# Kernel optimization log

Hardware: AMD Instinct MI355X
Metric: run time of the kernel (lower is better)

## Reference

```python
import jax, jax.numpy as jnp
import numpy as np

EPS = 1e-5

def group_norm(x, gamma, beta, groups):
    # x: (B, C, D, H, W)
    B, C = x.shape[0], x.shape[1]
    xr = x.reshape(B, groups, C // groups, -1)
    mean = xr.mean(axis=(2, 3), keepdims=True)
    var = xr.var(axis=(2, 3), keepdims=True)
    xn = ((xr - mean) * jax.lax.rsqrt(var + EPS)).reshape(x.shape)
    return xn * gamma[None, :, None, None, None] + beta[None, :, None, None, None]

def setup_inputs() -> dict:
    key = jax.random.key(0)
    ks = jax.random.split(key, 8)
    B, Ccls = 2, 32
    D = H = W = 64
    s = 0.05
    return {
        "x": jax.random.normal(ks[0], (B, 768, 8, 8, 8), jnp.float32),
        "out": jax.random.normal(ks[1], (B, 48, D, H, W), jnp.float32),
        "task_encoding": jax.random.normal(ks[2], (Ccls, 256, 1, 1, 1), jnp.float32),
        "gn1_g": jnp.ones((768,), jnp.float32),
        "gn1_b": jnp.zeros((768,), jnp.float32),
        "gap_w": jax.random.normal(ks[3], (256, 768), jnp.float32) * s,
        "gap_b": jnp.zeros((256,), jnp.float32),
        "ctrl_w": jax.random.normal(ks[4], (153, 512), jnp.float32) * s,
        "ctrl_b": jnp.zeros((153,), jnp.float32),
        "gn2_g": jnp.ones((48,), jnp.float32),
        "gn2_b": jnp.zeros((48,), jnp.float32),
        "pre_w": jax.random.normal(ks[5], (8, 48), jnp.float32) * s,
        "pre_b": jnp.zeros((8,), jnp.float32),
    }

def reference(x, out, task_encoding, gn1_g, gn1_b, gap_w, gap_b, ctrl_w, ctrl_b,
              gn2_g, gn2_b, pre_w, pre_b):
    B = x.shape[0]
    Ccls = task_encoding.shape[0]
    # GAP branch: GroupNorm(16,768) -> ReLU -> global avg pool -> 1x1x1 conv 768->256
    h = jax.nn.relu(group_norm(x, gn1_g, gn1_b, 16))
    pooled = h.mean(axis=(2, 3, 4))                       # (B, 768)
    x_feat = pooled @ gap_w.T + gap_b                     # (B, 256)
    # Controller: per (batch, class) params from concat(x_feat, task_encoding)
    te = task_encoding.reshape(Ccls, -1)                  # (Ccls, 256)
    params = (jnp.einsum('pf,bf->bp', ctrl_w[:, :256], x_feat)[:, None, :]
              + jnp.einsum('pf,cf->cp', ctrl_w[:, 256:], te)[None, :, :]
              + ctrl_b)                                   # (B, Ccls, 153)
    w1 = params[..., 0:64].reshape(B, Ccls, 8, 8)
    w2 = params[..., 64:128].reshape(B, Ccls, 8, 8)
    w3 = params[..., 128:136].reshape(B, Ccls, 1, 8)
    b1 = params[..., 136:144]
    b2 = params[..., 144:152]
    b3 = params[..., 152:153]
    # precls branch: GroupNorm(16,48) -> ReLU -> 1x1x1 conv 48->8
    g = jax.nn.relu(group_norm(out, gn2_g, gn2_b, 16))
    h0 = jnp.einsum('oc,bcdhw->bodhw', pre_w, g) + pre_b[None, :, None, None, None]
    # Dynamic per-class head: 8->8->8->1 pointwise MLP with ReLU between layers
    t = jax.nn.relu(jnp.einsum('bcij,bjdhw->bcidhw', w1, h0) + b1[..., None, None, None])
    t = jax.nn.relu(jnp.einsum('bcij,bcjdhw->bcidhw', w2, t) + b2[..., None, None, None])
    logits = jnp.einsum('bcij,bcjdhw->bcidhw', w3, t) + b3[..., None, None, None]
    # (B, Ccls, 1, D, H, W) -> (B, Ccls, D, H, W)
    return logits[:, :, 0]
```

## Files before the change

kernel.cpp:

```cpp
#include <hip/hip_runtime.h>

constexpr int NCLS = 32;

constexpr int WS_POOL = 64;
constexpr int WS_XF  = 1600;
constexpr int WS_PAR = 2112;
constexpr int WS_P2  = 11904;

__device__ __forceinline__ float wred(float v) {
#pragma unroll
  for (int off = 32; off > 0; off >>= 1) v += __shfl_down(v, off, 64);
  return v;
}

__device__ __forceinline__ float2 fma2(float w, float2 v, float2 a) {
  a.x = fmaf(w, v.x, a.x); a.y = fmaf(w, v.y, a.y);
  return a;
}
__device__ __forceinline__ float2 relu2(float2 a) {
  a.x = fmaxf(a.x, 0.f); a.y = fmaxf(a.y, 0.f);
  return a;
}
__device__ __forceinline__ float2 bcast2(float v) { return make_float2(v, v); }

__global__ void k1_stats(const float* __restrict__ x, const float* __restrict__ oin,
                         const float* __restrict__ g1, const float* __restrict__ b1,
                         float* __restrict__ ws) {
  int t = threadIdx.x;
  int wid = t >> 6, lane = t & 63;
  __shared__ float red[8];
  if (blockIdx.x < 768) {
    int blk = blockIdx.x;
    const float4* p = reinterpret_cast<const float4*>(oin + (size_t)blk * 32768);
    float s = 0.f, s2 = 0.f;
#pragma unroll
    for (int k = 0; k < 32; ++k) {
      float4 v = p[k * 256 + t];
      s  += v.x + v.y + v.z + v.w;
      s2 += v.x*v.x + v.y*v.y + v.z*v.z + v.w*v.w;
    }
    s = wred(s); s2 = wred(s2);
    if (lane == 0) { red[wid*2] = s; red[wid*2+1] = s2; }
    __syncthreads();
    if (t == 0) {
      ws[WS_P2 + blk*2]   = red[0]+red[2]+red[4]+red[6];
      ws[WS_P2 + blk*2+1] = red[1]+red[3]+red[5]+red[7];
    }
  } else {
    int g = blockIdx.x - 768;
    __shared__ float mstat[2];
    const float4* p = reinterpret_cast<const float4*>(x + g * 24576);
    float s = 0.f, s2 = 0.f;
#pragma unroll
    for (int k = 0; k < 24; ++k) {
      float4 v = p[k * 256 + t];
      s  += v.x + v.y + v.z + v.w;
      s2 += v.x*v.x + v.y*v.y + v.z*v.z + v.w*v.w;
    }
    s = wred(s); s2 = wred(s2);
    if (lane == 0) { red[wid*2] = s; red[wid*2+1] = s2; }
    __syncthreads();
    if (t == 0) {
      float S  = red[0]+red[2]+red[4]+red[6];
      float S2 = red[1]+red[3]+red[5]+red[7];
      float mean = S * (1.f/24576.f);
      float var  = S2 * (1.f/24576.f) - mean*mean;
      mstat[0] = mean; mstat[1] = rsqrtf(var + 1e-5f);
    }
    __syncthreads();
    float mean = mstat[0], rstd = mstat[1];
#pragma unroll
    for (int k = 0; k < 12; ++k) {
      int i = k*4 + wid;
      int c = (g & 15) * 48 + i;
      float sc = rstd * g1[c];
      float sh = b1[c] - mean * sc;
      const float* q = x + g * 24576 + i * 512;
      float acc = 0.f;
#pragma unroll
      for (int j = 0; j < 8; ++j)
        acc += fmaxf(fmaf(q[lane + j*64], sc, sh), 0.f);
      acc = wred(acc);
      if (lane == 0) ws[WS_POOL + (g >> 4) * 768 + c] = acc * (1.f/512.f);
    }
  }
}

__global__ void k2_xfeat(const float* __restrict__ gapw, const float* __restrict__ gapb,
                         float* __restrict__ ws) {
  int wid = threadIdx.x >> 6, lane = threadIdx.x & 63;
  int idx = blockIdx.x * 4 + wid;
  int b = idx >> 8, o = idx & 255;
  const float* pw = gapw + o * 768;
  const float* pp = ws + WS_POOL + b * 768;
  float s = 0.f;
#pragma unroll
  for (int i = 0; i < 12; ++i) {
    int cc = lane + i*64;
    s += pw[cc] * pp[cc];
  }
  s = wred(s);
  if (lane == 0) ws[WS_XF + idx] = s + gapb[o];
}

__global__ void k3_params(const float* __restrict__ cw, const float* __restrict__ cb,
                          const float* __restrict__ te, float* __restrict__ ws) {
  int wid = threadIdx.x >> 6, lane = threadIdx.x & 63;
  int e = blockIdx.x * 4 + wid;
  int b = e / (NCLS * 153);
  int r = e % (NCLS * 153);
  int c = r / 153, p = r % 153;
  const float* w  = cw + p * 512;
  const float* xf = ws + WS_XF + b * 256;
  const float* tv = te + c * 256;
  float s = 0.f;
#pragma unroll
  for (int i = 0; i < 4; ++i) {
    int f = lane + i*64;
    s += w[f] * xf[f] + w[256 + f] * tv[f];
  }
  s = wred(s);
  if (lane == 0) ws[WS_PAR + e] = s + cb[p];
}

__global__ __launch_bounds__(256) void k4_main(const float* __restrict__ oin,
                                               const float* __restrict__ prew,
                                               const float* __restrict__ preb,
                                               const float* __restrict__ g2,
                                               const float* __restrict__ b2,
                                               const float* __restrict__ ws,
                                               float* __restrict__ out) {
  __shared__ __align__(16) float prewT[384];
  __shared__ float2 ssl[48];
  __shared__ float ms[64];
  int t = threadIdx.x;
  int b    = blockIdx.x >> 9;
  int tile = blockIdx.x & 511;

  if (t < 32) {
    float S = 0.f, S2 = 0.f;
#pragma unroll
    for (int k = 0; k < 24; ++k) {
      S  += ws[WS_P2 + (t*24 + k)*2];
      S2 += ws[WS_P2 + (t*24 + k)*2 + 1];
    }
    float mean = S * (1.f/786432.f);
    float var  = S2 * (1.f/786432.f) - mean*mean;
    ms[t*2] = mean; ms[t*2+1] = rsqrtf(var + 1e-5f);
  }
  if (t < 128) {
#pragma unroll
    for (int k = 0; k < 3; ++k) {
      int i = t + k*128;
      prewT[(i % 48) * 8 + (i / 48)] = prew[i];
    }
  }
  __syncthreads();
  if (t < 48) {
    int grp = (b << 4) + t / 3;
    float mean = ms[grp*2], rstd = ms[grp*2+1];
    float sc = rstd * g2[t];
    ssl[t] = make_float2(sc, b2[t] - mean * sc);
  }
  __syncthreads();

  const float2* ip2 = reinterpret_cast<const float2*>(oin)
                      + (size_t)b * 48 * 131072 + tile*256 + t;
  const float4* pT4 = reinterpret_cast<const float4*>(prewT);
  float2 h0[8];
#pragma unroll
  for (int o = 0; o < 8; ++o) h0[o] = bcast2(preb[o]);
#pragma unroll 8
  for (int c = 0; c < 48; ++c) {
    float2 v = ip2[(size_t)c * 131072];
    float2 ss = ssl[c];
    float2 g = relu2(make_float2(fmaf(v.x, ss.x, ss.y), fmaf(v.y, ss.x, ss.y)));
    float4 w0 = pT4[c*2], w1 = pT4[c*2+1];
    h0[0] = fma2(w0.x, g, h0[0]);
    h0[1] = fma2(w0.y, g, h0[1]);
    h0[2] = fma2(w0.z, g, h0[2]);
    h0[3] = fma2(w0.w, g, h0[3]);
    h0[4] = fma2(w1.x, g, h0[4]);
    h0[5] = fma2(w1.y, g, h0[5]);
    h0[6] = fma2(w1.z, g, h0[6]);
    h0[7] = fma2(w1.w, g, h0[7]);
  }

  const float* __restrict__ Wb = ws + WS_PAR + (size_t)b * NCLS * 153;
  float2* op2 = reinterpret_cast<float2*>(out)
                + (size_t)b * NCLS * 131072 + tile*256 + t;
#pragma unroll 1
  for (int cls = 0; cls < NCLS; ++cls) {
    const float* Wc = Wb + cls * 153;
    float2 t1[8];
#pragma unroll
    for (int i = 0; i < 8; ++i) {
      float2 a = bcast2(Wc[136 + i]);
#pragma unroll
      for (int j = 0; j < 8; ++j) a = fma2(Wc[i*8 + j], h0[j], a);
      t1[i] = relu2(a);
    }
    float2 lg = bcast2(Wc[152]);
#pragma unroll
    for (int i = 0; i < 8; ++i) {
      float2 a = bcast2(Wc[144 + i]);
#pragma unroll
      for (int j = 0; j < 8; ++j) a = fma2(Wc[64 + i*8 + j], t1[j], a);
      a = relu2(a);
      lg = fma2(Wc[128 + i], a, lg);
    }
    op2[(size_t)cls * 131072] = lg;
  }
}

extern "C" void kernel_launch(void* const* d_in, const int* in_sizes, int n_in,
                              void* d_out, int out_size, void* d_ws, size_t ws_size,
                              hipStream_t stream) {
  const float* x    = (const float*)d_in[0];
  const float* oin  = (const float*)d_in[1];
  const float* te   = (const float*)d_in[2];
  const float* g1   = (const float*)d_in[3];
  const float* b1   = (const float*)d_in[4];
  const float* gapw = (const float*)d_in[5];
  const float* gapb = (const float*)d_in[6];
  const float* cw   = (const float*)d_in[7];
  const float* cb   = (const float*)d_in[8];
  const float* g2   = (const float*)d_in[9];
  const float* b2   = (const float*)d_in[10];
  const float* prew = (const float*)d_in[11];
  const float* preb = (const float*)d_in[12];
  float* ws  = (float*)d_ws;
  float* out = (float*)d_out;

  hipLaunchKernelGGL(k1_stats,  dim3(800),  dim3(256), 0, stream, x, oin, g1, b1, ws);
  hipLaunchKernelGGL(k2_xfeat,  dim3(128),  dim3(256), 0, stream, gapw, gapb, ws);
  hipLaunchKernelGGL(k3_params, dim3(2448), dim3(256), 0, stream, cw, cb, te, ws);
  hipLaunchKernelGGL(k4_main,   dim3(1024), dim3(256), 0, stream, oin, prew, preb, g2, b2, ws, out);
}
```

Before: 332.2 us.

## Process eight voxels per thread with packed FMA and split classes across blocks

The main kernel now has each thread handle 8 voxels (two float4 loads per channel) and uses packed two-wide FMA/max builtins, which should map to packed fp32 instructions. The 32 classes are split into two halves across blocks, and each block stages its 16 classes' dynamic weights in shared memory so they can be read as float4. The grid shrinks to 512 blocks. The intent is to raise arithmetic density and issue efficiency in the compute-bound MLP head. The cost is that the precls conv is recomputed twice per tile, register pressure rises, and there are fewer blocks.

Result: faster. 281.8 us (-15.2%).

```diff
diff --git a/kernel.cpp b/kernel.cpp
--- a/kernel.cpp
+++ b/kernel.cpp
@@ -7,21 +7,23 @@
 constexpr int WS_PAR = 2112;
 constexpr int WS_P2  = 11904;
 
+typedef float f2 __attribute__((ext_vector_type(2)));
+
 __device__ __forceinline__ float wred(float v) {
 #pragma unroll
   for (int off = 32; off > 0; off >>= 1) v += __shfl_down(v, off, 64);
   return v;
 }
 
-__device__ __forceinline__ float2 fma2(float w, float2 v, float2 a) {
-  a.x = fmaf(w, v.x, a.x); a.y = fmaf(w, v.y, a.y);
-  return a;
-}
-__device__ __forceinline__ float2 relu2(float2 a) {
-  a.x = fmaxf(a.x, 0.f); a.y = fmaxf(a.y, 0.f);
-  return a;
-}
-__device__ __forceinline__ float2 bcast2(float v) { return make_float2(v, v); }
+__device__ __forceinline__ f2 pfma(float w, f2 v, f2 a) {
+  return __builtin_elementwise_fma((f2)w, v, a);
+}
+__device__ __forceinline__ f2 paff(f2 v, float sc, float sh) {
+  return __builtin_elementwise_fma(v, (f2)sc, (f2)sh);
+}
+__device__ __forceinline__ f2 prelu(f2 a) {
+  return __builtin_elementwise_max(a, (f2)0.f);
+}
 
 __global__ void k1_stats(const float* __restrict__ x, const float* __restrict__ oin,
                          const float* __restrict__ g1, const float* __restrict__ b1,
@@ -130,12 +132,15 @@
                                                const float* __restrict__ b2,
                                                const float* __restrict__ ws,
                                                float* __restrict__ out) {
+  __shared__ __align__(16) float Wl[16 * 160];
   __shared__ __align__(16) float prewT[384];
   __shared__ float2 ssl[48];
   __shared__ float ms[64];
   int t = threadIdx.x;
-  int b    = blockIdx.x >> 9;
-  int tile = blockIdx.x & 511;
+  int b    = blockIdx.x >> 8;
+  int rem  = blockIdx.x & 255;
+  int tile = rem >> 1;
+  int cls0 = (rem & 1) << 4;
 
   if (t < 32) {
     float S = 0.f, S2 = 0.f;
@@ -154,6 +159,12 @@
       int i = t + k*128;
       prewT[(i % 48) * 8 + (i / 48)] = prew[i];
     }
+  }
+  {
+    const float* wsrc = ws + WS_PAR + (size_t)(b * NCLS + cls0) * 153;
+#pragma unroll 4
+    for (int cc = 0; cc < 16; ++cc)
+      if (t < 153) Wl[cc*160 + t] = wsrc[cc*153 + t];
   }
   __syncthreads();
   if (t < 48) {
@@ -164,52 +175,85 @@
   }
   __syncthreads();
 
-  const float2* ip2 = reinterpret_cast<const float2*>(oin)
-                      + (size_t)b * 48 * 131072 + tile*256 + t;
+  const float4* ip4 = reinterpret_cast<const float4*>(oin)
+                      + (size_t)b * 48 * 65536 + tile*512 + t;
   const float4* pT4 = reinterpret_cast<const float4*>(prewT);
-  float2 h0[8];
-#pragma unroll
-  for (int o = 0; o < 8; ++o) h0[o] = bcast2(preb[o]);
+  f2 h0[8][4];
+#pragma unroll
+  for (int o = 0; o < 8; ++o) {
+    float pb = preb[o];
+#pragma unroll
+    for (int p = 0; p < 4; ++p) h0[o][p] = (f2)pb;
+  }
 #pragma unroll 8
   for (int c = 0; c < 48; ++c) {
-    float2 v = ip2[(size_t)c * 131072];
+    float4 va = ip4[(size_t)c * 65536];
+    float4 vb = ip4[(size_t)c * 65536 + 256];
     float2 ss = ssl[c];
-    float2 g = relu2(make_float2(fmaf(v.x, ss.x, ss.y), fmaf(v.y, ss.x, ss.y)));
+    f2 g[4];
+    g[0] = prelu(paff((f2){va.x, va.y}, ss.x, ss.y));
+    g[1] = prelu(paff((f2){va.z, va.w}, ss.x, ss.y));
+    g[2] = prelu(paff((f2){vb.x, vb.y}, ss.x, ss.y));
+    g[3] = prelu(paff((f2){vb.z, vb.w}, ss.x, ss.y));
     float4 w0 = pT4[c*2], w1 = pT4[c*2+1];
-    h0[0] = fma2(w0.x, g, h0[0]);
-    h0[1] = fma2(w0.y, g, h0[1]);
-    h0[2] = fma2(w0.z, g, h0[2]);
-    h0[3] = fma2(w0.w, g, h0[3]);
-    h0[4] = fma2(w1.x, g, h0[4]);
-    h0[5] = fma2(w1.y, g, h0[5]);
-    h0[6] = fma2(w1.z, g, h0[6]);
-    h0[7] = fma2(w1.w, g, h0[7]);
-  }
-
-  const float* __restrict__ Wb = ws + WS_PAR + (size_t)b * NCLS * 153;
-  float2* op2 = reinterpret_cast<float2*>(out)
-                + (size_t)b * NCLS * 131072 + tile*256 + t;
+    float wv[8] = {w0.x, w0.y, w0.z, w0.w, w1.x, w1.y, w1.z, w1.w};
+#pragma unroll
+    for (int o = 0; o < 8; ++o)
+#pragma unroll
+      for (int p = 0; p < 4; ++p) h0[o][p] = pfma(wv[o], g[p], h0[o][p]);
+  }
+
+  float4* op4 = reinterpret_cast<float4*>(out)
+                + (size_t)(b * NCLS + cls0) * 65536 + tile*512 + t;
 #pragma unroll 1
-  for (int cls = 0; cls < NCLS; ++cls) {
-    const float* Wc = Wb + cls * 153;
-    float2 t1[8];
+  for (int cls = 0; cls < 16; ++cls) {
+    const float*  Wc = Wl + cls * 160;
+    const float4* W4 = reinterpret_cast<const float4*>(Wc);
+    float4 b1q0 = W4[34], b1q1 = W4[35];
+    float4 b2q0 = W4[36], b2q1 = W4[37];
+    float4 w3q0 = W4[32], w3q1 = W4[33];
+    float b3v = Wc[152];
+    float b1arr[8] = {b1q0.x,b1q0.y,b1q0.z,b1q0.w,b1q1.x,b1q1.y,b1q1.z,b1q1.w};
+    float b2arr[8] = {b2q0.x,b2q0.y,b2q0.z,b2q0.w,b2q1.x,b2q1.y,b2q1.z,b2q1.w};
+    float w3arr[8] = {w3q0.x,w3q0.y,w3q0.z,w3q0.w,w3q1.x,w3q1.y,w3q1.z,w3q1.w};
+
+    f2 t1[8][4];
 #pragma unroll
     for (int i = 0; i < 8; ++i) {
-      float2 a = bcast2(Wc[136 + i]);
-#pragma unroll
-      for (int j = 0; j < 8; ++j) a = fma2(Wc[i*8 + j], h0[j], a);
-      t1[i] = relu2(a);
-    }
-    float2 lg = bcast2(Wc[152]);
+      float4 w0 = W4[i*2], w1 = W4[i*2+1];
+      float wv[8] = {w0.x, w0.y, w0.z, w0.w, w1.x, w1.y, w1.z, w1.w};
+      f2 a[4];
+#pragma unroll
+      for (int p = 0; p < 4; ++p) a[p] = (f2)b1arr[i];
+#pragma unroll
+      for (int j = 0; j < 8; ++j)
+#pragma unroll
+        for (int p = 0; p < 4; ++p) a[p] = pfma(wv[j], h0[j][p], a[p]);
+#pragma unroll
+      for (int p = 0; p < 4; ++p) t1[i][p] = prelu(a[p]);
+    }
+    f2 lg[4];
+#pragma unroll
+    for (int p = 0; p < 4; ++p) lg[p] = (f2)b3v;
 #pragma unroll
     for (int i = 0; i < 8; ++i) {
-      float2 a = bcast2(Wc[144 + i]);
-#pragma unroll
-      for (int j = 0; j < 8; ++j) a = fma2(Wc[64 + i*8 + j], t1[j], a);
-      a = relu2(a);
-      lg = fma2(Wc[128 + i], a, lg);
-    }
-    op2[(size_t)cls * 131072] = lg;
+      float4 w0 = W4[16 + i*2], w1 = W4[17 + i*2];
+      float wv[8] = {w0.x, w0.y, w0.z, w0.w, w1.x, w1.y, w1.z, w1.w};
+      f2 a[4];
+#pragma unroll
+      for (int p = 0; p < 4; ++p) a[p] = (f2)b2arr[i];
+#pragma unroll
+      for (int j = 0; j < 8; ++j)
+#pragma unroll
+        for (int p = 0; p < 4; ++p) a[p] = pfma(wv[j], t1[j][p], a[p]);
+#pragma unroll
+      for (int p = 0; p < 4; ++p) {
+        a[p] = prelu(a[p]);
+        lg[p] = pfma(w3arr[i], a[p], lg[p]);
+      }
+    }
+    op4[(size_t)cls * 65536]       = make_float4(lg[0].x, lg[0].y, lg[1].x, lg[1].y);
+    op4[(size_t)cls * 65536 + 256] = make_float4(lg[2].x, lg[2].y, lg[3].x, lg[3].y);
   }
 }
 
@@ -235,5 +279,5 @@
   hipLaunchKernelGGL(k1_stats,  dim3(800),  dim3(256), 0, stream, x, oin, g1, b1, ws);
   hipLaunchKernelGGL(k2_xfeat,  dim3(128),  dim3(256), 0, stream, gapw, gapb, ws);
   hipLaunchKernelGGL(k3_params, dim3(2448), dim3(256), 0, stream, cw, cb, te, ws);
-  hipLaunchKernelGGL(k4_main,   dim3(1024), dim3(256), 0, stream, oin, prew, preb, g2, b2, ws, out);
-}
+  hipLaunchKernelGGL(k4_main,   dim3(512),  dim3(256), 0, stream, oin, prew, preb, g2, b2, ws, out);
+}
```
